# Optimization experiments

Measured on AMD Instinct MI355X. Metric: run time of the kernel, lower is better.

## Reference

```python
import jax, jax.numpy as jnp
import numpy as np

KERNEL = 3
PAD = KERNEL // 2


def setup_inputs() -> dict:
    key = jax.random.key(0)
    k1, k2, k3, k4 = jax.random.split(key, 4)
    B, Cin, Cout, D = 2, 32, 64, 64
    x = jax.random.normal(k1, (B, Cin, D, D, D), dtype=jnp.float32)
    mask = jax.random.randint(k2, (B, D, D, D), 0, 2).astype(jnp.bool_)
    fan_in = Cin * KERNEL ** 3
    bound = 1.0 / np.sqrt(fan_in)
    weight = jax.random.uniform(k3, (Cout, Cin, KERNEL, KERNEL, KERNEL),
                                dtype=jnp.float32, minval=-bound, maxval=bound)
    bias = jax.random.uniform(k4, (Cout,), dtype=jnp.float32, minval=-bound, maxval=bound)
    return {"x": x, "mask": mask, "weight": weight, "bias": bias}


def reference(x, mask, weight, bias):
    # Dense conv3d with 'same' padding, then zero out unoccupied voxels
    # (the CUDA warp kernel only computes occupied voxels; others are 0).
    out = jax.lax.conv_general_dilated(
        x, weight,
        window_strides=(1, 1, 1),
        padding=[(PAD, PAD)] * 3,
        dimension_numbers=("NCDHW", "OIDHW", "NCDHW"),
    )
    out = out + bias[None, :, None, None, None]
    return out * mask[:, None, :, :, :].astype(out.dtype)
```

## Files before the change

### kernel.cpp

```cpp
#include <hip/hip_runtime.h>
#include <stdint.h>


#define DD 64
#define CIN 32
#define COUT 64

typedef __bf16 bf16x8 __attribute__((ext_vector_type(8)));
typedef float f32x16 __attribute__((ext_vector_type(16)));

#define ROW_B_    1056u
#define OCT_B     6336u
#define SLAB_B    25344u
#define PLANE_OCT (66u * ROW_B_)
#define XT_BYTES  ((size_t)2 * 64 * 4 * 66 * ROW_B_)
#define WPK_U16   (27 * 2 * 2 * 64 * 8)
#define WPK_BYTES ((size_t)WPK_U16 * 2)
#define ZP_BYTES  ((size_t)SLAB_B)
#define WS_NEEDED (XT_BYTES + WPK_BYTES + ZP_BYTES)
#define CONV_LDS  (3 * 25344)

__device__ __forceinline__ uint16_t f2bf(float f) {
    uint32_t u = __builtin_bit_cast(uint32_t, f);
    u += 0x7fffu + ((u >> 16) & 1u);
    return (uint16_t)(u >> 16);
}

__device__ __forceinline__ void gll16(const void* g, void* l) {
    __builtin_amdgcn_global_load_lds(
        (__attribute__((address_space(1))) void*)g,
        (__attribute__((address_space(3))) void*)l, 16, 0, 0);
}

__global__ void pack_weights(const float* __restrict__ w, uint16_t* __restrict__ wpk,
                             uint4* __restrict__ zp) {
    int flat = blockIdx.x * 256 + threadIdx.x;
    if (flat < WPK_U16) {
        int j   = flat & 7;
        int l   = (flat >> 3) & 63;
        int ct  = (flat >> 9) & 1;
        int cb  = (flat >> 10) & 1;
        int k27 = flat >> 11;
        int co = ct * 32 + (l & 31);
        int ci = cb * 16 + ((l >> 5) * 8) + j;
        wpk[flat] = f2bf(w[(co * CIN + ci) * 27 + k27]);
    } else if (flat - WPK_U16 < (int)(ZP_BYTES / 16)) {
        zp[flat - WPK_U16] = make_uint4(0, 0, 0, 0);
    }
}

__global__ __launch_bounds__(256)
void transpose_x(const float* __restrict__ x, uint16_t* __restrict__ xt) {
    __shared__ uint16_t tile[4 * 66 * 8];
    const int yy = blockIdx.x, z = blockIdx.y, b = blockIdx.z;
    const int y = yy - 1;
    const int t = threadIdx.x;
    uint4* dst0 = (uint4*)(xt + ((((size_t)(b * DD + z)) * 4 + 0) * 66 + yy) * (ROW_B_ / 2));
    const size_t oct_stride4 = PLANE_OCT / 16;

    if (y < 0 || y >= DD) {
        for (int i = t; i < 264; i += 256)
            dst0[(i / 66) * oct_stride4 + (i % 66)] = make_uint4(0, 0, 0, 0);
        return;
    }
    const int ci = t >> 3;
    const int xs = (t & 7) * 8;
    const float* src = x + ((((size_t)b * CIN + ci) * DD + z) * DD + y) * DD + xs;
    float4 v0 = *(const float4*)src;
    float4 v1 = *(const float4*)(src + 4);
    float vals[8] = {v0.x, v0.y, v0.z, v0.w, v1.x, v1.y, v1.z, v1.w};
    const int oct = ci >> 3, j = ci & 7;
#pragma unroll
    for (int e = 0; e < 8; ++e)
        tile[(oct * 66 + (xs + e + 1)) * 8 + j] = f2bf(vals[e]);
    if (t < 64) {
        const int o2 = t >> 4, s2 = ((t >> 3) & 1) ? 65 : 0, j2 = t & 7;
        tile[(o2 * 66 + s2) * 8 + j2] = 0;
    }
    __syncthreads();
    const uint4* t4 = (const uint4*)tile;
    for (int i = t; i < 264; i += 256)
        dst0[(i / 66) * oct_stride4 + (i % 66)] = t4[i];
}

__global__ __launch_bounds__(512, 4)
void conv_mfma(const uint16_t* __restrict__ xt, const uint16_t* __restrict__ wpk,
               const uint16_t* __restrict__ zp,
               const int* __restrict__ mask, const float* __restrict__ bias,
               float* __restrict__ out) {
    extern __shared__ __align__(16) unsigned char lds[];
    const int yq = blockIdx.x, z = blockIdx.y, b = blockIdx.z;
    const int y0 = yq * 4;
    const int tid = threadIdx.x;
    const int lane = tid & 63;
    const int w = __builtin_amdgcn_readfirstlane(tid >> 6);
    const int ct    = w & 1;
    const int xtile = (w >> 1) & 1;
    const int wy    = w >> 2;
    const int u = lane & 31;
    const int h = lane >> 5;
    const int xoff = xtile * 32;

    for (int r = w; r < 12; r += 8) {
        const int zr = r >> 2, oct = r & 3;
        const int zz = z - 1 + zr;
        const char* g = (zz >= 0 && zz < DD)
            ? (const char*)xt + ((((size_t)(b * DD + zz)) * 4 + oct) * 66 + y0) * ROW_B_
            : (const char*)zp + oct * OCT_B;
        const unsigned l = (unsigned)(zr * SLAB_B + oct * OCT_B);
#pragma unroll
        for (int c = 0; c < 6; ++c)
            gll16(g + c * 1024 + lane * 16, &lds[l + (unsigned)c * 1024u]);
        if (lane < 12) gll16(g + 6144 + lane * 16, &lds[l + 6144u]);
    }
    __syncthreads();

    f32x16 acc0 = {}, acc1 = {};

#pragma unroll
    for (int zr = 0; zr < 3; ++zr) {
#pragma unroll
        for (int cbp = 0; cbp < 2; ++cbp) {
            bf16x8 wf[9];
#pragma unroll
            for (int q = 0; q < 9; ++q)
                wf[q] = *(const bf16x8*)(wpk
                    + (size_t)(((zr * 9 + q) * 2 + cbp) * 2 + ct) * 512 + lane * 8);
            const unsigned ob = (unsigned)(zr * SLAB_B + (cbp * 2 + h) * OCT_B)
                              + (unsigned)(xoff + u) * 16u;
            bf16x8 bfc[3], bfn[3];
#pragma unroll
            for (int kx = 0; kx < 3; ++kx)
                bfc[kx] = *(const bf16x8*)&lds[ob + (unsigned)(2 * wy + 0) * ROW_B_ + kx * 16u];
#pragma unroll
            for (int t = 0; t < 4; ++t) {
                if (t < 3) {
#pragma unroll
                    for (int kx = 0; kx < 3; ++kx)
                        bfn[kx] = *(const bf16x8*)&lds[ob + (unsigned)(2 * wy + t + 1) * ROW_B_ + kx * 16u];
                }
#pragma unroll
                for (int kx = 0; kx < 3; ++kx) {
                    if (t <= 2)
                        acc0 = __builtin_amdgcn_mfma_f32_32x32x16_bf16(
                            wf[t * 3 + kx], bfc[kx], acc0, 0, 0, 0);
                    if (t >= 1)
                        acc1 = __builtin_amdgcn_mfma_f32_32x32x16_bf16(
                            wf[(t - 1) * 3 + kx], bfc[kx], acc1, 0, 0, 0);
                }
#pragma unroll
                for (int kx = 0; kx < 3; ++kx) bfc[kx] = bfn[kx];
            }
        }
    }

    const int ya = y0 + 2 * wy;
    const size_t mb = (((size_t)b * DD + z) * DD + ya) * DD + xoff + u;
    const float m0 = mask[mb]      ? 1.0f : 0.0f;
    const float m1 = mask[mb + DD] ? 1.0f : 0.0f;
#pragma unroll
    for (int r = 0; r < 16; ++r) {
        const int co = ct * 32 + (r & 3) + 8 * (r >> 2) + 4 * h;
        const float bs = bias[co];
        const size_t o = (((size_t)(b * COUT + co) * DD + z) * DD + ya) * DD + xoff + u;
        out[o]      = (acc0[r] + bs) * m0;
        out[o + DD] = (acc1[r] + bs) * m1;
    }
}

#define CI_BLK 16
__global__ __launch_bounds__(256, 2)
void sparse_conv3d_f32(const float* __restrict__ x,
                       const int* __restrict__ mask,
                       const float* __restrict__ weight,
                       const float* __restrict__ bias,
                       float* __restrict__ out) {
    __shared__ float lds[9 * CI_BLK * 66];
    const int y = blockIdx.x, z = blockIdx.y, b = blockIdx.z;
    const int lane = threadIdx.x & 63;
    const int wave = __builtin_amdgcn_readfirstlane(threadIdx.x >> 6);
    float acc[16];
#pragma unroll
    for (int j = 0; j < 16; ++j) acc[j] = 0.0f;
    const int co0 = wave * 16;
    const float* wbase = weight + (size_t)co0 * (CIN * 27);
    for (int cbl = 0; cbl < 2; ++cbl) {
        if (cbl) __syncthreads();
        for (int i = wave; i < 9 * CI_BLK; i += 4) {
            const int r = i >> 4, ci_l = i & 15;
            const int zz = z + (r / 3) - 1, yy = y + (r % 3) - 1;
            const int ci = cbl * CI_BLK + ci_l;
            float v = 0.0f;
            if (zz >= 0 && zz < DD && yy >= 0 && yy < DD)
                v = x[((((size_t)b * CIN + ci) * DD + zz) * DD + yy) * DD + lane];
            float* row = &lds[(size_t)i * 66];
            row[1 + lane] = v;
            if (lane == 0) { row[0] = 0.0f; row[65] = 0.0f; }
        }
        __syncthreads();
        for (int ci_l = 0; ci_l < CI_BLK; ++ci_l) {
            const int ci = cbl * CI_BLK + ci_l;
#pragma unroll
            for (int kz = 0; kz < 3; ++kz) {
#pragma unroll
                for (int ky = 0; ky < 3; ++ky) {
                    const int r = kz * 3 + ky;
                    const float* xrow = &lds[(size_t)(r * CI_BLK + ci_l) * 66 + lane];
                    const float xv0 = xrow[0], xv1 = xrow[1], xv2 = xrow[2];
                    const float* wp = wbase + ci * 27 + kz * 9 + ky * 3;
#pragma unroll
                    for (int j = 0; j < 16; ++j) {
                        acc[j] += wp[(size_t)j * (CIN * 27) + 0] * xv0
                                + wp[(size_t)j * (CIN * 27) + 1] * xv1
                                + wp[(size_t)j * (CIN * 27) + 2] * xv2;
                    }
                }
            }
        }
    }
    const float m = mask[(((size_t)b * DD + z) * DD + y) * DD + lane] ? 1.0f : 0.0f;
#pragma unroll
    for (int j = 0; j < 16; ++j) {
        const int co = co0 + j;
        out[((((size_t)b * COUT + co) * DD + z) * DD + y) * DD + lane] = (acc[j] + bias[co]) * m;
    }
}
#undef CI_BLK

extern "C" void kernel_launch(void* const* d_in, const int* in_sizes, int n_in,
                              void* d_out, int out_size, void* d_ws, size_t ws_size,
                              hipStream_t stream) {
    const float* x    = (const float*)d_in[0];
    const int*   mask = (const int*)d_in[1];
    const float* w    = (const float*)d_in[2];
    const float* bias = (const float*)d_in[3];
    float*       out  = (float*)d_out;

    if (ws_size < WS_NEEDED) {
        sparse_conv3d_f32<<<dim3(DD, DD, 2), 256, 0, stream>>>(x, mask, w, bias, out);
        return;
    }

    uint16_t* xt  = (uint16_t*)d_ws;
    uint16_t* wpk = (uint16_t*)((char*)d_ws + XT_BYTES);
    uint16_t* zp  = (uint16_t*)((char*)d_ws + XT_BYTES + WPK_BYTES);

    pack_weights<<<(WPK_U16 + (int)(ZP_BYTES / 16) + 255) / 256, 256, 0, stream>>>(w, wpk, (uint4*)zp);
    transpose_x<<<dim3(66, DD, 2), 256, 0, stream>>>(x, xt);
    conv_mfma<<<dim3(16, DD, 2), 512, CONV_LDS, stream>>>(xt, wpk, zp, mask, bias, out);
}
```

Before: 92.47 us.

## Give each wave four output rows and double-buffer weight fragments in conv MFMA

The conv kernel drops from 8 to 4 waves per block, and each wave now accumulates four output y-rows instead of two. Each weight fragment set loaded from global memory is reused across more MFMAs, and each LDS B-fragment row feeds up to three accumulators. The weights for the next (z-plane, channel-block) phase are prefetched into a second register buffer while the current phase computes. The cost is more accumulator and weight registers per thread and fewer waves per block, which can lower occupancy and latency hiding.

Result: slower. 99.12 us (+7.2%).

```diff
diff --git a/kernel.cpp b/kernel.cpp
--- a/kernel.cpp
+++ b/kernel.cpp
@@ -83,7 +83,7 @@
         dst0[(i / 66) * oct_stride4 + (i % 66)] = t4[i];
 }
 
-__global__ __launch_bounds__(512, 4)
+__global__ __launch_bounds__(256, 2)
 void conv_mfma(const uint16_t* __restrict__ xt, const uint16_t* __restrict__ wpk,
                const uint16_t* __restrict__ zp,
                const int* __restrict__ mask, const float* __restrict__ bias,
@@ -95,13 +95,12 @@
     const int lane = tid & 63;
     const int w = __builtin_amdgcn_readfirstlane(tid >> 6);
     const int ct    = w & 1;
-    const int xtile = (w >> 1) & 1;
-    const int wy    = w >> 2;
+    const int xtile = w >> 1;
     const int u = lane & 31;
     const int h = lane >> 5;
     const int xoff = xtile * 32;
 
-    for (int r = w; r < 12; r += 8) {
+    for (int r = w; r < 12; r += 4) {
         const int zr = r >> 2, oct = r & 3;
         const int zz = z - 1 + zr;
         const char* g = (zz >= 0 && zz < DD)
@@ -113,58 +112,58 @@
             gll16(g + c * 1024 + lane * 16, &lds[l + (unsigned)c * 1024u]);
         if (lane < 12) gll16(g + 6144 + lane * 16, &lds[l + 6144u]);
     }
+
+    bf16x8 wfA[9], wfB[9];
+#define LOAD_WF(DST, zr_, cb_)                                                     \
+    _Pragma("unroll") for (int q = 0; q < 9; ++q)                                  \
+        DST[q] = *(const bf16x8*)(wpk                                              \
+            + (size_t)((((zr_) * 9 + q) * 2 + (cb_)) * 2 + ct) * 512 + lane * 8);
+
+    LOAD_WF(wfA, 0, 0)
     __syncthreads();
 
-    f32x16 acc0 = {}, acc1 = {};
-
-#pragma unroll
-    for (int zr = 0; zr < 3; ++zr) {
-#pragma unroll
-        for (int cbp = 0; cbp < 2; ++cbp) {
-            bf16x8 wf[9];
-#pragma unroll
-            for (int q = 0; q < 9; ++q)
-                wf[q] = *(const bf16x8*)(wpk
-                    + (size_t)(((zr * 9 + q) * 2 + cbp) * 2 + ct) * 512 + lane * 8);
-            const unsigned ob = (unsigned)(zr * SLAB_B + (cbp * 2 + h) * OCT_B)
-                              + (unsigned)(xoff + u) * 16u;
-            bf16x8 bfc[3], bfn[3];
-#pragma unroll
-            for (int kx = 0; kx < 3; ++kx)
-                bfc[kx] = *(const bf16x8*)&lds[ob + (unsigned)(2 * wy + 0) * ROW_B_ + kx * 16u];
-#pragma unroll
-            for (int t = 0; t < 4; ++t) {
-                if (t < 3) {
-#pragma unroll
-                    for (int kx = 0; kx < 3; ++kx)
-                        bfn[kx] = *(const bf16x8*)&lds[ob + (unsigned)(2 * wy + t + 1) * ROW_B_ + kx * 16u];
-                }
-#pragma unroll
-                for (int kx = 0; kx < 3; ++kx) {
-                    if (t <= 2)
-                        acc0 = __builtin_amdgcn_mfma_f32_32x32x16_bf16(
-                            wf[t * 3 + kx], bfc[kx], acc0, 0, 0, 0);
-                    if (t >= 1)
-                        acc1 = __builtin_amdgcn_mfma_f32_32x32x16_bf16(
-                            wf[(t - 1) * 3 + kx], bfc[kx], acc1, 0, 0, 0);
-                }
-#pragma unroll
-                for (int kx = 0; kx < 3; ++kx) bfc[kx] = bfn[kx];
-            }
-        }
-    }
-
-    const int ya = y0 + 2 * wy;
-    const size_t mb = (((size_t)b * DD + z) * DD + ya) * DD + xoff + u;
-    const float m0 = mask[mb]      ? 1.0f : 0.0f;
-    const float m1 = mask[mb + DD] ? 1.0f : 0.0f;
+    f32x16 acc[4] = {};
+
+#define PHASE(zr_, cb_, WFC, WFN, pzr, pcb, DOPRE)                                 \
+    {   const unsigned ob = (unsigned)((zr_) * SLAB_B + ((cb_) * 2 + h) * OCT_B)   \
+                          + (unsigned)(xoff + u) * 16u;                            \
+        if (DOPRE) { LOAD_WF(WFN, pzr, pcb) }                                      \
+        _Pragma("unroll") for (int t = 0; t < 6; ++t) {                            \
+            bf16x8 bf[3];                                                          \
+            _Pragma("unroll") for (int kx = 0; kx < 3; ++kx)                       \
+                bf[kx] = *(const bf16x8*)&lds[ob + (unsigned)t * ROW_B_ + kx * 16u];\
+            _Pragma("unroll") for (int ly = 0; ly < 4; ++ly) {                     \
+                const int ky = t - ly;                                             \
+                if (ky >= 0 && ky < 3) {                                           \
+                    _Pragma("unroll") for (int kx = 0; kx < 3; ++kx)               \
+                        acc[ly] = __builtin_amdgcn_mfma_f32_32x32x16_bf16(         \
+                            WFC[ky * 3 + kx], bf[kx], acc[ly], 0, 0, 0);           \
+                }                                                                  \
+            }                                                                      \
+        }                                                                          \
+    }
+
+    PHASE(0, 0, wfA, wfB, 0, 1, 1)
+    PHASE(0, 1, wfB, wfA, 1, 0, 1)
+    PHASE(1, 0, wfA, wfB, 1, 1, 1)
+    PHASE(1, 1, wfB, wfA, 2, 0, 1)
+    PHASE(2, 0, wfA, wfB, 2, 1, 1)
+    PHASE(2, 1, wfB, wfA, 0, 0, 0)
+#undef PHASE
+#undef LOAD_WF
+
+    const size_t mb = (((size_t)b * DD + z) * DD + y0) * DD + xoff + u;
+    float m[4];
+#pragma unroll
+    for (int ly = 0; ly < 4; ++ly) m[ly] = mask[mb + ly * DD] ? 1.0f : 0.0f;
 #pragma unroll
     for (int r = 0; r < 16; ++r) {
         const int co = ct * 32 + (r & 3) + 8 * (r >> 2) + 4 * h;
         const float bs = bias[co];
-        const size_t o = (((size_t)(b * COUT + co) * DD + z) * DD + ya) * DD + xoff + u;
-        out[o]      = (acc0[r] + bs) * m0;
-        out[o + DD] = (acc1[r] + bs) * m1;
+        const size_t o = (((size_t)(b * COUT + co) * DD + z) * DD + y0) * DD + xoff + u;
+#pragma unroll
+        for (int ly = 0; ly < 4; ++ly)
+            out[o + ly * DD] = (acc[ly][r] + bs) * m[ly];
     }
 }
 
@@ -247,5 +246,5 @@
 
     pack_weights<<<(WPK_U16 + (int)(ZP_BYTES / 16) + 255) / 256, 256, 0, stream>>>(w, wpk, (uint4*)zp);
     transpose_x<<<dim3(66, DD, 2), 256, 0, stream>>>(x, xt);
-    conv_mfma<<<dim3(16, DD, 2), 512, CONV_LDS, stream>>>(xt, wpk, zp, mask, bias, out);
-}
+    conv_mfma<<<dim3(16, DD, 2), 256, CONV_LDS, stream>>>(xt, wpk, zp, mask, bias, out);
+}
```

## Halve conv block to 4 waves with 4 output rows each and split-channel LDS staging

Applied to the files above, without the earlier changes.

The MFMA conv block shrinks from 8 waves to 4. Each wave now accumulates all 4 output rows in four accumulators, so it reuses the same 9 weight fragments and each loaded LDS row across up to 3 output rows. The input slab is staged in two halves by channel octet pair, which halves the LDS footprint and lets more blocks reside per CU. The cost is an extra barrier and a reload phase per block, more accumulator registers per wave, and fewer waves per block to hide latency.

Result: slower. 94.91 us (+2.6%).

```diff
diff --git a/kernel.cpp b/kernel.cpp
--- a/kernel.cpp
+++ b/kernel.cpp
@@ -11,14 +11,14 @@
 
 #define ROW_B_    1056u
 #define OCT_B     6336u
-#define SLAB_B    25344u
+#define SLAB2_B   12672u
 #define PLANE_OCT (66u * ROW_B_)
 #define XT_BYTES  ((size_t)2 * 64 * 4 * 66 * ROW_B_)
 #define WPK_U16   (27 * 2 * 2 * 64 * 8)
 #define WPK_BYTES ((size_t)WPK_U16 * 2)
-#define ZP_BYTES  ((size_t)SLAB_B)
+#define ZP_BYTES  ((size_t)(4u * OCT_B))
 #define WS_NEEDED (XT_BYTES + WPK_BYTES + ZP_BYTES)
-#define CONV_LDS  (3 * 25344)
+#define CONV_LDS  (3 * 12672)
 
 __device__ __forceinline__ uint16_t f2bf(float f) {
     uint32_t u = __builtin_bit_cast(uint32_t, f);
@@ -83,7 +83,7 @@
         dst0[(i / 66) * oct_stride4 + (i % 66)] = t4[i];
 }
 
-__global__ __launch_bounds__(512, 4)
+__global__ __launch_bounds__(256, 4)
 void conv_mfma(const uint16_t* __restrict__ xt, const uint16_t* __restrict__ wpk,
                const uint16_t* __restrict__ zp,
                const int* __restrict__ mask, const float* __restrict__ bias,
@@ -95,76 +95,73 @@
     const int lane = tid & 63;
     const int w = __builtin_amdgcn_readfirstlane(tid >> 6);
     const int ct    = w & 1;
-    const int xtile = (w >> 1) & 1;
-    const int wy    = w >> 2;
+    const int xtile = w >> 1;
     const int u = lane & 31;
     const int h = lane >> 5;
     const int xoff = xtile * 32;
 
-    for (int r = w; r < 12; r += 8) {
-        const int zr = r >> 2, oct = r & 3;
-        const int zz = z - 1 + zr;
-        const char* g = (zz >= 0 && zz < DD)
-            ? (const char*)xt + ((((size_t)(b * DD + zz)) * 4 + oct) * 66 + y0) * ROW_B_
-            : (const char*)zp + oct * OCT_B;
-        const unsigned l = (unsigned)(zr * SLAB_B + oct * OCT_B);
-#pragma unroll
-        for (int c = 0; c < 6; ++c)
-            gll16(g + c * 1024 + lane * 16, &lds[l + (unsigned)c * 1024u]);
-        if (lane < 12) gll16(g + 6144 + lane * 16, &lds[l + 6144u]);
-    }
-    __syncthreads();
-
-    f32x16 acc0 = {}, acc1 = {};
-
-#pragma unroll
-    for (int zr = 0; zr < 3; ++zr) {
-#pragma unroll
-        for (int cbp = 0; cbp < 2; ++cbp) {
+    f32x16 acc[4] = {};
+
+#pragma unroll
+    for (int cbsel = 0; cbsel < 2; ++cbsel) {
+        if (cbsel) __syncthreads();
+
+        for (int r = w; r < 6; r += 4) {
+            const int zr = r >> 1, o2 = r & 1;
+            const int oct = cbsel * 2 + o2;
+            const int zz = z - 1 + zr;
+            const char* g = (zz >= 0 && zz < DD)
+                ? (const char*)xt + ((((size_t)(b * DD + zz)) * 4 + oct) * 66 + y0) * ROW_B_
+                : (const char*)zp + oct * OCT_B;
+            const unsigned l = (unsigned)(zr * SLAB2_B + o2 * OCT_B);
+#pragma unroll
+            for (int c = 0; c < 6; ++c)
+                gll16(g + c * 1024 + lane * 16, &lds[l + (unsigned)c * 1024u]);
+            if (lane < 12) gll16(g + 6144 + lane * 16, &lds[l + 6144u]);
+        }
+        __syncthreads();
+
+#pragma unroll
+        for (int zr = 0; zr < 3; ++zr) {
             bf16x8 wf[9];
 #pragma unroll
             for (int q = 0; q < 9; ++q)
                 wf[q] = *(const bf16x8*)(wpk
-                    + (size_t)(((zr * 9 + q) * 2 + cbp) * 2 + ct) * 512 + lane * 8);
-            const unsigned ob = (unsigned)(zr * SLAB_B + (cbp * 2 + h) * OCT_B)
+                    + (size_t)(((zr * 9 + q) * 2 + cbsel) * 2 + ct) * 512 + lane * 8);
+            const unsigned ob = (unsigned)(zr * SLAB2_B + h * OCT_B)
                               + (unsigned)(xoff + u) * 16u;
-            bf16x8 bfc[3], bfn[3];
-#pragma unroll
-            for (int kx = 0; kx < 3; ++kx)
-                bfc[kx] = *(const bf16x8*)&lds[ob + (unsigned)(2 * wy + 0) * ROW_B_ + kx * 16u];
-#pragma unroll
-            for (int t = 0; t < 4; ++t) {
-                if (t < 3) {
-#pragma unroll
-                    for (int kx = 0; kx < 3; ++kx)
-                        bfn[kx] = *(const bf16x8*)&lds[ob + (unsigned)(2 * wy + t + 1) * ROW_B_ + kx * 16u];
+#pragma unroll
+            for (int t = 0; t < 6; ++t) {
+                bf16x8 bf[3];
+#pragma unroll
+                for (int kx = 0; kx < 3; ++kx)
+                    bf[kx] = *(const bf16x8*)&lds[ob + (unsigned)t * ROW_B_ + kx * 16u];
+#pragma unroll
+                for (int ly = 0; ly < 4; ++ly) {
+                    const int ky = t - ly;
+                    if (ky >= 0 && ky < 3) {
+#pragma unroll
+                        for (int kx = 0; kx < 3; ++kx)
+                            acc[ly] = __builtin_amdgcn_mfma_f32_32x32x16_bf16(
+                                wf[ky * 3 + kx], bf[kx], acc[ly], 0, 0, 0);
+                    }
                 }
-#pragma unroll
-                for (int kx = 0; kx < 3; ++kx) {
-                    if (t <= 2)
-                        acc0 = __builtin_amdgcn_mfma_f32_32x32x16_bf16(
-                            wf[t * 3 + kx], bfc[kx], acc0, 0, 0, 0);
-                    if (t >= 1)
-                        acc1 = __builtin_amdgcn_mfma_f32_32x32x16_bf16(
-                            wf[(t - 1) * 3 + kx], bfc[kx], acc1, 0, 0, 0);
-                }
-#pragma unroll
-                for (int kx = 0; kx < 3; ++kx) bfc[kx] = bfn[kx];
             }
         }
     }
 
-    const int ya = y0 + 2 * wy;
-    const size_t mb = (((size_t)b * DD + z) * DD + ya) * DD + xoff + u;
-    const float m0 = mask[mb]      ? 1.0f : 0.0f;
-    const float m1 = mask[mb + DD] ? 1.0f : 0.0f;
+    const size_t mb = (((size_t)b * DD + z) * DD + y0) * DD + xoff + u;
+    float m[4];
+#pragma unroll
+    for (int ly = 0; ly < 4; ++ly) m[ly] = mask[mb + ly * DD] ? 1.0f : 0.0f;
 #pragma unroll
     for (int r = 0; r < 16; ++r) {
         const int co = ct * 32 + (r & 3) + 8 * (r >> 2) + 4 * h;
         const float bs = bias[co];
-        const size_t o = (((size_t)(b * COUT + co) * DD + z) * DD + ya) * DD + xoff + u;
-        out[o]      = (acc0[r] + bs) * m0;
-        out[o + DD] = (acc1[r] + bs) * m1;
+        const size_t o = (((size_t)(b * COUT + co) * DD + z) * DD + y0) * DD + xoff + u;
+#pragma unroll
+        for (int ly = 0; ly < 4; ++ly)
+            out[o + ly * DD] = (acc[ly][r] + bs) * m[ly];
     }
 }
 
@@ -247,5 +244,5 @@
 
     pack_weights<<<(WPK_U16 + (int)(ZP_BYTES / 16) + 255) / 256, 256, 0, stream>>>(w, wpk, (uint4*)zp);
     transpose_x<<<dim3(66, DD, 2), 256, 0, stream>>>(x, xt);
-    conv_mfma<<<dim3(16, DD, 2), 512, CONV_LDS, stream>>>(xt, wpk, zp, mask, bias, out);
-}
+    conv_mfma<<<dim3(16, DD, 2), 256, CONV_LDS, stream>>>(xt, wpk, zp, mask, bias, out);
+}
```
